# Performance work log

Measured on AMD Instinct MI355X. Metric: run time of the kernel, lower is better.

Reference implementation:

```python
import jax, jax.numpy as jnp
import numpy as np

EPS = 1e-5

def _ln(x, g, b):
    m = jnp.mean(x, -1, keepdims=True)
    v = jnp.mean((x - m) ** 2, -1, keepdims=True)
    return (x - m) * jax.lax.rsqrt(v + EPS) * g + b

def _lstm(x, Wih, Whh, bih, bhh):
    # x: [B, T, D]; torch gate order i, f, g, o; h0 = c0 = 0
    B = x.shape[0]
    H = Whh.shape[1]
    h0 = jnp.zeros((B, H), x.dtype)
    c0 = jnp.zeros((B, H), x.dtype)
    bias = bih + bhh
    def step(carry, xt):
        h, c = carry
        gates = xt @ Wih.T + h @ Whh.T + bias  # [B, 4H]
        i, f, g, o = jnp.split(gates, 4, axis=-1)
        c = jax.nn.sigmoid(f) * c + jax.nn.sigmoid(i) * jnp.tanh(g)
        h = jax.nn.sigmoid(o) * jnp.tanh(c)
        return (h, c), h
    _, hs = jax.lax.scan(step, (h0, c0), jnp.swapaxes(x, 0, 1))
    return jnp.swapaxes(hs, 0, 1)  # [B, T, H]

def setup_inputs() -> dict:
    key = jax.random.key(0)
    ks = jax.random.split(key, 20)
    N, C, F, T = 4, 64, 256, 256
    D, H = 128, 32  # LSTM in/out
    s = 0.05
    inp = {
        "inputs": jax.random.normal(ks[0], (N, C, F, T, 2), jnp.float32),
        "ln1_g": jnp.ones((D,), jnp.float32), "ln1_b": jnp.zeros((D,), jnp.float32),
        "Wih_q": s * jax.random.normal(ks[1], (4 * H, D), jnp.float32),
        "Whh_q": s * jax.random.normal(ks[2], (4 * H, H), jnp.float32),
        "bih_q": s * jax.random.normal(ks[3], (4 * H,), jnp.float32),
        "bhh_q": s * jax.random.normal(ks[4], (4 * H,), jnp.float32),
        "Wih_k": s * jax.random.normal(ks[5], (4 * H, D), jnp.float32),
        "Whh_k": s * jax.random.normal(ks[6], (4 * H, H), jnp.float32),
        "bih_k": s * jax.random.normal(ks[7], (4 * H,), jnp.float32),
        "bhh_k": s * jax.random.normal(ks[8], (4 * H,), jnp.float32),
        "Wih_v": s * jax.random.normal(ks[9], (4 * H, D), jnp.float32),
        "Whh_v": s * jax.random.normal(ks[10], (4 * H, H), jnp.float32),
        "bih_v": s * jax.random.normal(ks[11], (4 * H,), jnp.float32),
        "bhh_v": s * jax.random.normal(ks[12], (4 * H,), jnp.float32),
        "ln2_g": jnp.ones((H,), jnp.float32), "ln2_b": jnp.zeros((H,), jnp.float32),
        "Wr": s * jax.random.normal(ks[13], (C, H // 2), jnp.float32),
        "br": s * jax.random.normal(ks[14], (C,), jnp.float32),
        "Wi": s * jax.random.normal(ks[15], (C, H // 2), jnp.float32),
        "bi": s * jax.random.normal(ks[16], (C,), jnp.float32),
        "ln3_g": jnp.ones((C,), jnp.float32), "ln3_b": jnp.zeros((C,), jnp.float32),
        "prelu_a": jnp.full((1,), 0.25, jnp.float32),
    }
    return inp

def reference(inputs, ln1_g, ln1_b,
              Wih_q, Whh_q, bih_q, bhh_q,
              Wih_k, Whh_k, bih_k, bhh_k,
              Wih_v, Whh_v, bih_v, bhh_v,
              ln2_g, ln2_b, Wr, br, Wi, bi,
              ln3_g, ln3_b, prelu_a):
    N, C, F, T, ri = inputs.shape
    # [N,C,F,T,2] -> [N*F, T, C, 2] -> concat real/imag -> [N*F, T, 2C]
    x4 = jnp.transpose(inputs, (0, 2, 3, 1, 4)).reshape(N * F, T, C, ri)
    x = jnp.concatenate([x4[..., 0], x4[..., 1]], axis=-1)  # [B, T, 128]
    # Self_Attention_T_RICAT (single head)
    xn = _ln(x, ln1_g, ln1_b)
    q = _lstm(xn, Wih_q, Whh_q, bih_q, bhh_q)  # [B, T, 32]
    k = _lstm(xn, Wih_k, Whh_k, bih_k, bhh_k)
    v = _lstm(xn, Wih_v, Whh_v, bih_v, bhh_v)
    energy = jnp.einsum('btf,bsf->bts', q, k) / 4.0  # / 16**0.5
    mask = jnp.tril(jnp.ones((T, T), x.dtype))
    attn = jax.nn.softmax(energy * mask, axis=-1)  # multiplicative mask, as in source
    wv = jnp.einsum('bts,bsf->btf', attn, v)  # [B, T, 32]
    out = _ln(wv, ln2_g, ln2_b)
    # complex-valued linear fusion
    xr, xi = jnp.split(out, 2, axis=-1)  # [B, T, 16] each
    lr_r = xr @ Wr.T + br
    li_i = xi @ Wi.T + bi
    lr_i = xi @ Wr.T + br
    li_r = xr @ Wi.T + bi
    out_real = (lr_r - li_i).reshape(N, F, T, C).transpose(0, 3, 1, 2)  # [N,C,F,T]
    out_imag = (lr_i + li_r).reshape(N, F, T, C).transpose(0, 3, 1, 2)
    outs = jnp.stack([out_real, out_imag], axis=-1)  # [N,C,F,T,2]
    outs_t = jnp.swapaxes(outs, 1, 4)  # [N,2,F,T,C]
    outs = jnp.swapaxes(_ln(outs_t, ln3_g, ln3_b), 1, 4)
    outs = jnp.where(outs >= 0, outs, prelu_a[0] * outs)  # PReLU (eval mode, dropout=identity)
    return outs + inputs
```

## Files before the change

### kernel.cpp

```cpp
#include <hip/hip_runtime.h>
#include <hip/hip_bf16.h>
#include <stddef.h>


typedef __bf16 bf16x8 __attribute__((ext_vector_type(8)));
typedef float f32x4 __attribute__((ext_vector_type(4)));

__device__ __forceinline__ ushort f2bf(float x) {
    uint u = __builtin_bit_cast(uint, x);
    uint r = (u + 0x7fffu + ((u >> 16) & 1u)) >> 16;
    return (ushort)r;
}

__device__ __forceinline__ float fsig(float x) {
    return __builtin_amdgcn_rcpf(1.f + __expf(-x));
}
__device__ __forceinline__ float ftanh(float x) {
    return 1.f - 2.f * __builtin_amdgcn_rcpf(__expf(2.f * x) + 1.f);
}
__device__ __forceinline__ float wredsum(float v) {
#pragma unroll
    for (int off = 32; off; off >>= 1) v += __shfl_xor(v, off);
    return v;
}
__device__ __forceinline__ float hredsum(float v) {
#pragma unroll
    for (int off = 16; off; off >>= 1) v += __shfl_xor(v, off);
    return v;
}

__global__ __launch_bounds__(256) void k_prep(const float* __restrict__ in,
                                              const float* __restrict__ g1,
                                              const float* __restrict__ b1,
                                              ushort* __restrict__ xn) {
    __shared__ float xl[32][129];
    const int n = blockIdx.z, f = blockIdx.y, t0 = blockIdx.x * 32;
    const int tid = threadIdx.x;
    const int c = tid >> 2, q = tid & 3;
    const float* src = in + ((size_t)(n * 64 + c) * 256 + f) * 512 + t0 * 2 + q * 16;
#pragma unroll
    for (int e = 0; e < 4; ++e) {
        float4 v4 = *(const float4*)(src + e * 4);
        int dt = q * 8 + e * 2;
        xl[dt][c]          = v4.x;
        xl[dt][c + 64]     = v4.y;
        xl[dt + 1][c]      = v4.z;
        xl[dt + 1][c + 64] = v4.w;
    }
    __syncthreads();
    const int lane = tid & 63, w = tid >> 6;
    const int b = n * 256 + f;
#pragma unroll 1
    for (int r = 0; r < 8; ++r) {
        int dt = w * 8 + r;
        float a = xl[dt][lane], bb = xl[dt][lane + 64];
        float s = wredsum(a + bb);
        float mean = s * 0.0078125f;
        float da = a - mean, db = bb - mean;
        float var = wredsum(da * da + db * db) * 0.0078125f;
        float inv = __builtin_amdgcn_rsqf(var + 1e-5f);
        size_t base = ((size_t)b * 256 + (t0 + dt)) * 128;
        xn[base + lane]      = f2bf(da * inv * g1[lane] + b1[lane]);
        xn[base + lane + 64] = f2bf(db * inv * g1[lane + 64] + b1[lane + 64]);
    }
}

__global__ __launch_bounds__(256) void k_gemm(const ushort* __restrict__ xn,
                                              const float* __restrict__ Wq,
                                              const float* __restrict__ Wk,
                                              const float* __restrict__ Wv,
                                              const float* __restrict__ bihq, const float* __restrict__ bhhq,
                                              const float* __restrict__ bihk, const float* __restrict__ bhhk,
                                              const float* __restrict__ bihv, const float* __restrict__ bhhv,
                                              ushort* __restrict__ gx) {
    __shared__ ushort a_lds[128 * 136];
    __shared__ ushort w_lds[128 * 136];
    const int tid = threadIdx.x;
    const int m0 = blockIdx.x * 128;

#pragma unroll
    for (int p = 0; p < 8; ++p) {
        int idx = p * 256 + tid;
        int r = idx >> 4, c = idx & 15;
        *(uint4*)&a_lds[r * 136 + c * 8] =
            *(const uint4*)(xn + (size_t)(m0 + r) * 128 + c * 8);
    }

    const int w = tid >> 6, lane = tid & 63;
    const int wr = w >> 1, wc = w & 1;
    const int row16 = lane & 15, koct = lane >> 4;

#pragma unroll 1
    for (int l = 0; l < 3; ++l) {
        const float* W   = (l == 0) ? Wq   : (l == 1) ? Wk   : Wv;
        const float* bih = (l == 0) ? bihq : (l == 1) ? bihk : bihv;
        const float* bhh = (l == 0) ? bhhq : (l == 1) ? bhhk : bhhv;
        __syncthreads();
#pragma unroll
        for (int p = 0; p < 8; ++p) {
            int idx = p * 256 + tid;
            int r = idx >> 4, c = idx & 15;
            const float* wp = W + (size_t)r * 128 + c * 8;
            float4 wa = *(const float4*)wp;
            float4 wb = *(const float4*)(wp + 4);
            union { ushort u[8]; uint4 v; } pk;
            pk.u[0] = f2bf(wa.x); pk.u[1] = f2bf(wa.y); pk.u[2] = f2bf(wa.z); pk.u[3] = f2bf(wa.w);
            pk.u[4] = f2bf(wb.x); pk.u[5] = f2bf(wb.y); pk.u[6] = f2bf(wb.z); pk.u[7] = f2bf(wb.w);
            *(uint4*)&w_lds[r * 136 + c * 8] = pk.v;
        }
        __syncthreads();

        f32x4 acc[4][4];
#pragma unroll
        for (int mi = 0; mi < 4; ++mi)
#pragma unroll
            for (int ni = 0; ni < 4; ++ni) acc[mi][ni] = (f32x4){0.f, 0.f, 0.f, 0.f};

#pragma unroll
        for (int ki = 0; ki < 4; ++ki) {
            bf16x8 af[4], bfr[4];
#pragma unroll
            for (int mi = 0; mi < 4; ++mi)
                af[mi] = *(const bf16x8*)&a_lds[(wr * 64 + mi * 16 + row16) * 136 + ki * 32 + koct * 8];
#pragma unroll
            for (int ni = 0; ni < 4; ++ni)
                bfr[ni] = *(const bf16x8*)&w_lds[(wc * 64 + ni * 16 + row16) * 136 + ki * 32 + koct * 8];
#pragma unroll
            for (int mi = 0; mi < 4; ++mi)
#pragma unroll
                for (int ni = 0; ni < 4; ++ni)
                    acc[mi][ni] = __builtin_amdgcn_mfma_f32_16x16x32_bf16(af[mi], bfr[ni], acc[mi][ni], 0, 0, 0);
        }

#pragma unroll
        for (int ni = 0; ni < 4; ++ni) {
            int g = wc * 64 + ni * 16 + row16;
            float bsv = bih[g] + bhh[g];
            int j = g & 31, gi = g >> 5;
            int s = j * 4 + gi;
#pragma unroll
            for (int mi = 0; mi < 4; ++mi)
#pragma unroll
                for (int q = 0; q < 4; ++q) {
                    size_t m = (size_t)m0 + wr * 64 + mi * 16 + koct * 4 + q;
                    gx[m * 384 + l * 128 + s] = f2bf(acc[mi][ni][q] + bsv);
                }
        }
    }
}

__global__ __launch_bounds__(128, 1) void k_lstm(const ushort* __restrict__ gx,
                                                 const float* __restrict__ Whq,
                                                 const float* __restrict__ Whk,
                                                 const float* __restrict__ Whv,
                                                 ushort* __restrict__ qkv) {
    __shared__ ushort H[2][16][40];
    const int tid = threadIdx.x;
    const int w = tid >> 6, lane = tid & 63;
    const int r16 = lane & 15, koct = lane >> 4;
    const int l = blockIdx.x >> 6, bgrp = blockIdx.x & 63;
    const int b = bgrp * 16 + r16;
    const float* Wh = (l == 0) ? Whq : (l == 1) ? Whk : Whv;

    bf16x8 wf[4];
#pragma unroll
    for (int gg = 0; gg < 4; ++gg) {
        int g = 4 * w + gg;
        int jA = 8 * (r16 >> 2) + g;
        int giA = r16 & 3;
        const float* wp = Wh + (size_t)(giA * 32 + jA) * 32 + koct * 8;
        float4 wa = *(const float4*)wp;
        float4 wb = *(const float4*)(wp + 4);
        union { ushort u[8]; bf16x8 v; } pk;
        pk.u[0] = f2bf(wa.x); pk.u[1] = f2bf(wa.y); pk.u[2] = f2bf(wa.z); pk.u[3] = f2bf(wa.w);
        pk.u[4] = f2bf(wb.x); pk.u[5] = f2bf(wb.y); pk.u[6] = f2bf(wb.z); pk.u[7] = f2bf(wb.w);
        wf[gg] = pk.v;
    }

    const ushort* gp = gx + (size_t)b * 98304 + l * 128 + koct * 32 + w * 16;
    uint4 pf[4][2];
#pragma unroll
    for (int tt = 0; tt < 4; ++tt) {
        pf[tt][0] = *(const uint4*)(gp + (size_t)tt * 384);
        pf[tt][1] = *(const uint4*)(gp + (size_t)tt * 384 + 8);
    }

    for (int i = tid; i < 320; i += 128) ((uint*)&H[0][0][0])[i] = 0;
    __syncthreads();

    float cst[4] = {0.f, 0.f, 0.f, 0.f};
    ushort* outp = qkv + ((size_t)(l * 1024 + b)) * 8192 + koct * 8 + w * 4;

#pragma unroll 4
    for (int t = 0; t < 256; ++t) {
        const int sl = t & 3;
        const int p = t & 1;
        bf16x8 hf = *(const bf16x8*)&H[p][r16][koct * 8];

        uint u[8];
        u[0] = pf[sl][0].x; u[1] = pf[sl][0].y; u[2] = pf[sl][0].z; u[3] = pf[sl][0].w;
        u[4] = pf[sl][1].x; u[5] = pf[sl][1].y; u[6] = pf[sl][1].z; u[7] = pf[sl][1].w;
        pf[sl][0] = *(const uint4*)(gp + (size_t)(t + 4) * 384);
        pf[sl][1] = *(const uint4*)(gp + (size_t)(t + 4) * 384 + 8);

        f32x4 acc[4];
#pragma unroll
        for (int gg = 0; gg < 4; ++gg)
#pragma unroll
            for (int q = 0; q < 4; ++q) {
                int v = gg * 4 + q;
                uint w32 = u[v >> 1];
                acc[gg][q] = __builtin_bit_cast(float, (v & 1) ? (w32 & 0xffff0000u) : (w32 << 16));
            }
#pragma unroll
        for (int gg = 0; gg < 4; ++gg)
            acc[gg] = __builtin_amdgcn_mfma_f32_16x16x32_bf16(wf[gg], hf, acc[gg], 0, 0, 0);

        float hv[4];
#pragma unroll
        for (int gg = 0; gg < 4; ++gg) {
            float gi = acc[gg][0], gf = acc[gg][1], gg2 = acc[gg][2], go = acc[gg][3];
            float cN = fsig(gf) * cst[gg] + fsig(gi) * ftanh(gg2);
            cst[gg] = cN;
            hv[gg] = fsig(go) * ftanh(cN);
        }
        uint2 hp;
        __asm__ volatile("v_cvt_pk_bf16_f32 %0, %1, %2" : "=v"(hp.x) : "v"(hv[0]), "v"(hv[1]));
        __asm__ volatile("v_cvt_pk_bf16_f32 %0, %1, %2" : "=v"(hp.y) : "v"(hv[2]), "v"(hv[3]));
        *(uint2*)&H[p ^ 1][r16][koct * 8 + w * 4] = hp;
        *(uint2*)(outp + (size_t)t * 32) = hp;
        __syncthreads();
    }
}

__global__ __launch_bounds__(256) void k_attn(const ushort* __restrict__ qkvb,
                                              float* __restrict__ wvout) {
    __shared__ ushort k_sw[256 * 32];
    __shared__ ushort vt_sw[32 * 256];
    __shared__ ushort p_sw[4][16 * 256];
    const int tid = threadIdx.x, w = tid >> 6, lane = tid & 63;
    const int b = blockIdx.x;
    const ushort* qb = qkvb + (size_t)b * 8192;
    const ushort* kb = qkvb + 8388608 + (size_t)b * 8192;
    const ushort* vb = qkvb + 16777216 + (size_t)b * 8192;
#pragma unroll
    for (int p = 0; p < 4; ++p) {
        int idx = p * 256 + tid;
        int s = idx >> 2, cc = idx & 3;
        uint4 kv = *(const uint4*)(kb + s * 32 + cc * 8);
        int cK = cc ^ ((s >> 1) & 3);
        *(uint4*)&k_sw[s * 32 + cK * 8] = kv;
        uint4 vv = *(const uint4*)(vb + s * 32 + cc * 8);
        union { uint4 v; ushort u[8]; } un; un.v = vv;
#pragma unroll
        for (int e = 0; e < 8; ++e) {
            int row = cc * 8 + e;
            vt_sw[row * 256 + (((s >> 3) ^ (row & 7)) << 3) + (s & 7)] = un.u[e];
        }
    }
    __syncthreads();
    const int r16 = lane & 15, koct = lane >> 4;
    ushort* pw = p_sw[w];
    bf16x8 qf[4];
#pragma unroll
    for (int i = 0; i < 4; ++i) {
        int t = (w * 4 + i) * 16 + r16;
        qf[i] = *(const bf16x8*)(qb + t * 32 + koct * 8);
    }
#pragma unroll 1
    for (int i = 0; i < 4; ++i) {
        const int tb = (w * 4 + i) * 16;
        f32x4 acc[16];
#pragma unroll
        for (int st = 0; st < 16; ++st) acc[st] = (f32x4){0.f, 0.f, 0.f, 0.f};
#pragma unroll
        for (int st = 0; st < 16; ++st) {
            int s = st * 16 + r16;
            int cK = koct ^ ((s >> 1) & 3);
            bf16x8 kf = *(const bf16x8*)&k_sw[s * 32 + cK * 8];
            acc[st] = __builtin_amdgcn_mfma_f32_16x16x32_bf16(qf[i], kf, acc[st], 0, 0, 0);
        }
        float mx[4] = {-1e30f, -1e30f, -1e30f, -1e30f};
#pragma unroll
        for (int st = 0; st < 16; ++st) {
            int s = st * 16 + r16;
#pragma unroll
            for (int q = 0; q < 4; ++q) {
                int t = tb + koct * 4 + q;
                float v = (s <= t) ? acc[st][q] * 0.25f : 0.f;
                acc[st][q] = v;
                mx[q] = fmaxf(mx[q], v);
            }
        }
#pragma unroll
        for (int off = 1; off < 16; off <<= 1)
#pragma unroll
            for (int q = 0; q < 4; ++q) mx[q] = fmaxf(mx[q], __shfl_xor(mx[q], off));
        float sm[4] = {0.f, 0.f, 0.f, 0.f};
#pragma unroll
        for (int st = 0; st < 16; ++st)
#pragma unroll
            for (int q = 0; q < 4; ++q) {
                float p = __expf(acc[st][q] - mx[q]);
                acc[st][q] = p; sm[q] += p;
            }
#pragma unroll
        for (int off = 1; off < 16; off <<= 1)
#pragma unroll
            for (int q = 0; q < 4; ++q) sm[q] += __shfl_xor(sm[q], off);
        float rs[4];
#pragma unroll
        for (int q = 0; q < 4; ++q) rs[q] = __builtin_amdgcn_rcpf(sm[q]);
#pragma unroll
        for (int st = 0; st < 16; ++st) {
            int schunk = st * 2 + (r16 >> 3), sl = r16 & 7;
#pragma unroll
            for (int q = 0; q < 4; ++q) {
                int tl = koct * 4 + q;
                pw[tl * 256 + ((schunk ^ (tl & 7)) << 3) + sl] = f2bf(acc[st][q] * rs[q]);
            }
        }
        __asm__ volatile("s_waitcnt lgkmcnt(0)" ::: "memory");
        f32x4 oa[2];
        oa[0] = (f32x4){0.f, 0.f, 0.f, 0.f};
        oa[1] = (f32x4){0.f, 0.f, 0.f, 0.f};
#pragma unroll
        for (int ks = 0; ks < 8; ++ks) {
            int kc = ks * 4 + koct;
            bf16x8 pa = *(const bf16x8*)&pw[r16 * 256 + ((kc ^ (r16 & 7)) << 3)];
#pragma unroll
            for (int n = 0; n < 2; ++n) {
                int row = n * 16 + r16;
                bf16x8 vf = *(const bf16x8*)&vt_sw[row * 256 + ((kc ^ (row & 7)) << 3)];
                oa[n] = __builtin_amdgcn_mfma_f32_16x16x32_bf16(pa, vf, oa[n], 0, 0, 0);
            }
        }
#pragma unroll
        for (int n = 0; n < 2; ++n)
#pragma unroll
            for (int q = 0; q < 4; ++q)
                wvout[((size_t)b * 256 + tb + koct * 4 + q) * 32 + n * 16 + r16] = oa[n][q];
    }
}

__global__ __launch_bounds__(256) void k_post(const float* __restrict__ wv,
                                              const float* __restrict__ in,
                                              const float* __restrict__ g2,
                                              const float* __restrict__ b2,
                                              const float* __restrict__ Wr,
                                              const float* __restrict__ br,
                                              const float* __restrict__ Wi,
                                              const float* __restrict__ bi,
                                              const float* __restrict__ g3,
                                              const float* __restrict__ b3,
                                              const float* __restrict__ pa,
                                              float* __restrict__ outp) {
    __shared__ float xv[32][36];
    __shared__ float out_s[64][65];
    const int tid = threadIdx.x;
    const int n = blockIdx.z, f = blockIdx.y, t0 = blockIdx.x * 32;
    const int b = n * 256 + f;
    const int lane = tid & 63, w = tid >> 6;
    const int r16 = lane & 15, koct = lane >> 4;
    const int tt = w & 1, ri = w >> 1;

    for (int idx = tid; idx < 1024; idx += 256) {
        int dt = idx >> 5, j = idx & 31;
        xv[dt][j] = wv[((size_t)b * 256 + t0 + dt) * 32 + j];
    }

    bf16x8 bfr[4];
    float bias_v[4], g3v[4], b3v[4];
    const int kofs = (koct < 2) ? koct * 8 : (koct - 2) * 8;
#pragma unroll
    for (int ct = 0; ct < 4; ++ct) {
        int c = ct * 16 + r16;
        const float* srcW = (ri == 0) ? ((koct < 2) ? Wr : Wi)
                                      : ((koct < 2) ? Wi : Wr);
        float sgn = (ri == 0 && koct >= 2) ? -1.f : 1.f;
        float4 wa = *(const float4*)(srcW + c * 16 + kofs);
        float4 wb = *(const float4*)(srcW + c * 16 + kofs + 4);
        union { ushort u[8]; bf16x8 v; } pk;
        pk.u[0] = f2bf(sgn * wa.x); pk.u[1] = f2bf(sgn * wa.y);
        pk.u[2] = f2bf(sgn * wa.z); pk.u[3] = f2bf(sgn * wa.w);
        pk.u[4] = f2bf(sgn * wb.x); pk.u[5] = f2bf(sgn * wb.y);
        pk.u[6] = f2bf(sgn * wb.z); pk.u[7] = f2bf(sgn * wb.w);
        bfr[ct] = pk.v;
        bias_v[ct] = (ri == 0) ? (br[c] - bi[c]) : (br[c] + bi[c]);
        g3v[ct] = g3[c];
        b3v[ct] = b3[c];
    }
    const float alpha = pa[0];
    __syncthreads();

#pragma unroll 1
    for (int r = 0; r < 4; ++r) {
        int dt = w * 8 + r * 2 + (lane >> 5);
        int j = lane & 31;
        float v = xv[dt][j];
        float mean = hredsum(v) * 0.03125f;
        float d = v - mean;
        float var = hredsum(d * d) * 0.03125f;
        float inv = __builtin_amdgcn_rsqf(var + 1e-5f);
        xv[dt][j] = d * inv * g2[j] + b2[j];
    }
    __syncthreads();

    const float* xrow = &xv[tt * 16 + r16][koct * 8];
    float4 a0 = *(const float4*)xrow;
    float4 a1 = *(const float4*)(xrow + 4);
    uint4 ap;
    __asm__ volatile("v_cvt_pk_bf16_f32 %0, %1, %2" : "=v"(ap.x) : "v"(a0.x), "v"(a0.y));
    __asm__ volatile("v_cvt_pk_bf16_f32 %0, %1, %2" : "=v"(ap.y) : "v"(a0.z), "v"(a0.w));
    __asm__ volatile("v_cvt_pk_bf16_f32 %0, %1, %2" : "=v"(ap.z) : "v"(a1.x), "v"(a1.y));
    __asm__ volatile("v_cvt_pk_bf16_f32 %0, %1, %2" : "=v"(ap.w) : "v"(a1.z), "v"(a1.w));
    bf16x8 af = __builtin_bit_cast(bf16x8, ap);

    f32x4 acc[4];
#pragma unroll
    for (int ct = 0; ct < 4; ++ct) {
        acc[ct] = (f32x4){0.f, 0.f, 0.f, 0.f};
        acc[ct] = __builtin_amdgcn_mfma_f32_16x16x32_bf16(af, bfr[ct], acc[ct], 0, 0, 0);
    }

    float val[4][4];
    float s[4] = {0.f, 0.f, 0.f, 0.f}, sq[4] = {0.f, 0.f, 0.f, 0.f};
#pragma unroll
    for (int ct = 0; ct < 4; ++ct)
#pragma unroll
        for (int q = 0; q < 4; ++q) {
            float v = acc[ct][q] + bias_v[ct];
            val[ct][q] = v;
            s[q] += v;
            sq[q] += v * v;
        }
#pragma unroll
    for (int off = 1; off < 16; off <<= 1)
#pragma unroll
        for (int q = 0; q < 4; ++q) {
            s[q]  += __shfl_xor(s[q], off);
            sq[q] += __shfl_xor(sq[q], off);
        }
#pragma unroll
    for (int q = 0; q < 4; ++q) {
        float m = s[q] * 0.015625f;
        float var = fmaxf(sq[q] * 0.015625f - m * m, 0.f);
        float inv = __builtin_amdgcn_rsqf(var + 1e-5f);
        int t2 = (tt * 16 + koct * 4 + q) * 2 + ri;
#pragma unroll
        for (int ct = 0; ct < 4; ++ct) {
            float nv = (val[ct][q] - m) * inv * g3v[ct] + b3v[ct];
            nv = (nv >= 0.f) ? nv : alpha * nv;
            out_s[ct * 16 + r16][t2] = nv;
        }
    }
    __syncthreads();

    const int cc = tid >> 2, q = tid & 3;
    size_t base = ((size_t)(n * 64 + cc) * 256 + f) * 512 + t0 * 2 + q * 16;
#pragma unroll
    for (int e = 0; e < 4; ++e) {
        float4 iv = *(const float4*)(in + base + e * 4);
        int k0 = q * 16 + e * 4;
        float4 ov;
        ov.x = out_s[cc][k0]     + iv.x;
        ov.y = out_s[cc][k0 + 1] + iv.y;
        ov.z = out_s[cc][k0 + 2] + iv.z;
        ov.w = out_s[cc][k0 + 3] + iv.w;
        *(float4*)(outp + base + e * 4) = ov;
    }
}

extern "C" void kernel_launch(void* const* d_in, const int* in_sizes, int n_in,
                              void* d_out, int out_size, void* d_ws, size_t ws_size,
                              hipStream_t stream) {
    const float* in   = (const float*)d_in[0];
    const float* g1   = (const float*)d_in[1];
    const float* b1   = (const float*)d_in[2];
    const float* Wq   = (const float*)d_in[3];
    const float* Whq  = (const float*)d_in[4];
    const float* bihq = (const float*)d_in[5];
    const float* bhhq = (const float*)d_in[6];
    const float* Wk   = (const float*)d_in[7];
    const float* Whk  = (const float*)d_in[8];
    const float* bihk = (const float*)d_in[9];
    const float* bhhk = (const float*)d_in[10];
    const float* Wv   = (const float*)d_in[11];
    const float* Whv  = (const float*)d_in[12];
    const float* bihv = (const float*)d_in[13];
    const float* bhhv = (const float*)d_in[14];
    const float* g2   = (const float*)d_in[15];
    const float* b2   = (const float*)d_in[16];
    const float* Wr   = (const float*)d_in[17];
    const float* br   = (const float*)d_in[18];
    const float* Wi   = (const float*)d_in[19];
    const float* bi   = (const float*)d_in[20];
    const float* g3   = (const float*)d_in[21];
    const float* b3   = (const float*)d_in[22];
    const float* pa   = (const float*)d_in[23];
    float* outp = (float*)d_out;

    ushort* gxb  = (ushort*)d_ws;
    ushort* xnb  = (ushort*)((char*)d_ws + 201326592);
    ushort* qkvb = (ushort*)((char*)d_ws + 268435456);
    float*  wvb  = (float*)((char*)d_ws + 318767104);

    k_prep<<<dim3(8, 256, 4), dim3(256), 0, stream>>>(in, g1, b1, xnb);
    k_gemm<<<dim3(2048), dim3(256), 0, stream>>>(xnb, Wq, Wk, Wv,
                                                 bihq, bhhq, bihk, bhhk, bihv, bhhv, gxb);
    k_lstm<<<dim3(192), dim3(128), 0, stream>>>(gxb, Whq, Whk, Whv, qkvb);
    k_attn<<<dim3(1024), dim3(256), 0, stream>>>(qkvb, wvb);
    k_post<<<dim3(8, 256, 4), dim3(256), 0, stream>>>(wvb, in, g2, b2,
                                                      Wr, br, Wi, bi, g3, b3, pa, outp);
}
```

Measured before the change: 474.6 us.

## Run each LSTM block as a single wave, keeping hidden state in registers

The recurrent LSTM kernel drops from two waves per block to one. Each lane now handles eight gate groups instead of four, and the gate permutation in the input-projection GEMM is reordered so that a lane's MFMA output lines up directly with the B-operand layout for the next step. This lets the hidden state stay in registers and removes the per-timestep LDS write, LDS read and __syncthreads from the serial loop. In exchange each wave does twice the MFMA and transcendental work per step, with more registers and fewer waves in flight.

```diff
diff --git a/kernel.cpp b/kernel.cpp
--- a/kernel.cpp
+++ b/kernel.cpp
@@ -137,7 +137,7 @@
             int g = wc * 64 + ni * 16 + row16;
             float bsv = bih[g] + bhh[g];
             int j = g & 31, gi = g >> 5;
-            int s = j * 4 + gi;
+            int s = (j >> 3) * 32 + (j & 7) * 4 + gi;
 #pragma unroll
             for (int mi = 0; mi < 4; ++mi)
 #pragma unroll
@@ -149,87 +149,89 @@
     }
 }
 
-__global__ __launch_bounds__(128, 1) void k_lstm(const ushort* __restrict__ gx,
-                                                 const float* __restrict__ Whq,
-                                                 const float* __restrict__ Whk,
-                                                 const float* __restrict__ Whv,
-                                                 ushort* __restrict__ qkv) {
-    __shared__ ushort H[2][16][40];
-    const int tid = threadIdx.x;
-    const int w = tid >> 6, lane = tid & 63;
+__global__ __launch_bounds__(64, 1) void k_lstm(const ushort* __restrict__ gx,
+                                                const float* __restrict__ Whq,
+                                                const float* __restrict__ Whk,
+                                                const float* __restrict__ Whv,
+                                                ushort* __restrict__ qkv) {
+    const int lane = threadIdx.x & 63;
     const int r16 = lane & 15, koct = lane >> 4;
     const int l = blockIdx.x >> 6, bgrp = blockIdx.x & 63;
     const int b = bgrp * 16 + r16;
     const float* Wh = (l == 0) ? Whq : (l == 1) ? Whk : Whv;
 
-    bf16x8 wf[4];
-#pragma unroll
-    for (int gg = 0; gg < 4; ++gg) {
-        int g = 4 * w + gg;
-        int jA = 8 * (r16 >> 2) + g;
-        int giA = r16 & 3;
+    bf16x8 wf[8];
+#pragma unroll
+    for (int g = 0; g < 8; ++g) {
+        int P = g * 16 + r16;
+        int jA = 8 * ((P >> 2) & 3) + (P >> 4);
+        int giA = P & 3;
         const float* wp = Wh + (size_t)(giA * 32 + jA) * 32 + koct * 8;
         float4 wa = *(const float4*)wp;
         float4 wb = *(const float4*)(wp + 4);
         union { ushort u[8]; bf16x8 v; } pk;
         pk.u[0] = f2bf(wa.x); pk.u[1] = f2bf(wa.y); pk.u[2] = f2bf(wa.z); pk.u[3] = f2bf(wa.w);
         pk.u[4] = f2bf(wb.x); pk.u[5] = f2bf(wb.y); pk.u[6] = f2bf(wb.z); pk.u[7] = f2bf(wb.w);
-        wf[gg] = pk.v;
-    }
-
-    const ushort* gp = gx + (size_t)b * 98304 + l * 128 + koct * 32 + w * 16;
-    uint4 pf[4][2];
-#pragma unroll
-    for (int tt = 0; tt < 4; ++tt) {
-        pf[tt][0] = *(const uint4*)(gp + (size_t)tt * 384);
-        pf[tt][1] = *(const uint4*)(gp + (size_t)tt * 384 + 8);
-    }
-
-    for (int i = tid; i < 320; i += 128) ((uint*)&H[0][0][0])[i] = 0;
-    __syncthreads();
-
-    float cst[4] = {0.f, 0.f, 0.f, 0.f};
-    ushort* outp = qkv + ((size_t)(l * 1024 + b)) * 8192 + koct * 8 + w * 4;
+        wf[g] = pk.v;
+    }
+
+    const ushort* gp = gx + (size_t)b * 98304 + l * 128 + koct * 32;
+    uint4 pf[4][4];
+#pragma unroll
+    for (int tt = 0; tt < 4; ++tt)
+#pragma unroll
+        for (int i = 0; i < 4; ++i)
+            pf[tt][i] = *(const uint4*)(gp + (size_t)tt * 384 + i * 8);
+
+    float cst[8] = {0.f, 0.f, 0.f, 0.f, 0.f, 0.f, 0.f, 0.f};
+    uint4 z4 = make_uint4(0, 0, 0, 0);
+    bf16x8 hf = __builtin_bit_cast(bf16x8, z4);
+    ushort* outp = qkv + ((size_t)(l * 1024 + b)) * 8192 + koct * 8;
 
 #pragma unroll 4
     for (int t = 0; t < 256; ++t) {
         const int sl = t & 3;
-        const int p = t & 1;
-        bf16x8 hf = *(const bf16x8*)&H[p][r16][koct * 8];
-
-        uint u[8];
-        u[0] = pf[sl][0].x; u[1] = pf[sl][0].y; u[2] = pf[sl][0].z; u[3] = pf[sl][0].w;
-        u[4] = pf[sl][1].x; u[5] = pf[sl][1].y; u[6] = pf[sl][1].z; u[7] = pf[sl][1].w;
-        pf[sl][0] = *(const uint4*)(gp + (size_t)(t + 4) * 384);
-        pf[sl][1] = *(const uint4*)(gp + (size_t)(t + 4) * 384 + 8);
-
-        f32x4 acc[4];
-#pragma unroll
-        for (int gg = 0; gg < 4; ++gg)
+        uint u[16];
+#pragma unroll
+        for (int i = 0; i < 4; ++i) {
+            u[4 * i]     = pf[sl][i].x;
+            u[4 * i + 1] = pf[sl][i].y;
+            u[4 * i + 2] = pf[sl][i].z;
+            u[4 * i + 3] = pf[sl][i].w;
+        }
+        int tn = (t + 4 < 256) ? t + 4 : 255;
+#pragma unroll
+        for (int i = 0; i < 4; ++i)
+            pf[sl][i] = *(const uint4*)(gp + (size_t)tn * 384 + i * 8);
+
+        f32x4 acc[8];
+#pragma unroll
+        for (int g = 0; g < 8; ++g)
 #pragma unroll
             for (int q = 0; q < 4; ++q) {
-                int v = gg * 4 + q;
+                int v = g * 4 + q;
                 uint w32 = u[v >> 1];
-                acc[gg][q] = __builtin_bit_cast(float, (v & 1) ? (w32 & 0xffff0000u) : (w32 << 16));
+                acc[g][q] = __builtin_bit_cast(float, (v & 1) ? (w32 & 0xffff0000u) : (w32 << 16));
             }
 #pragma unroll
-        for (int gg = 0; gg < 4; ++gg)
-            acc[gg] = __builtin_amdgcn_mfma_f32_16x16x32_bf16(wf[gg], hf, acc[gg], 0, 0, 0);
-
-        float hv[4];
-#pragma unroll
-        for (int gg = 0; gg < 4; ++gg) {
-            float gi = acc[gg][0], gf = acc[gg][1], gg2 = acc[gg][2], go = acc[gg][3];
-            float cN = fsig(gf) * cst[gg] + fsig(gi) * ftanh(gg2);
-            cst[gg] = cN;
-            hv[gg] = fsig(go) * ftanh(cN);
-        }
-        uint2 hp;
+        for (int g = 0; g < 8; ++g)
+            acc[g] = __builtin_amdgcn_mfma_f32_16x16x32_bf16(wf[g], hf, acc[g], 0, 0, 0);
+
+        float hv[8];
+#pragma unroll
+        for (int g = 0; g < 8; ++g) {
+            float gi = acc[g][0], gf = acc[g][1], gg = acc[g][2], go = acc[g][3];
+            float cN = fsig(gf) * cst[g] + fsig(gi) * ftanh(gg);
+            cst[g] = cN;
+            hv[g] = fsig(go) * ftanh(cN);
+        }
+        uint4 hp;
         __asm__ volatile("v_cvt_pk_bf16_f32 %0, %1, %2" : "=v"(hp.x) : "v"(hv[0]), "v"(hv[1]));
         __asm__ volatile("v_cvt_pk_bf16_f32 %0, %1, %2" : "=v"(hp.y) : "v"(hv[2]), "v"(hv[3]));
-        *(uint2*)&H[p ^ 1][r16][koct * 8 + w * 4] = hp;
-        *(uint2*)(outp + (size_t)t * 32) = hp;
-        __syncthreads();
+        __asm__ volatile("v_cvt_pk_bf16_f32 %0, %1, %2" : "=v"(hp.z) : "v"(hv[4]), "v"(hv[5]));
+        __asm__ volatile("v_cvt_pk_bf16_f32 %0, %1, %2" : "=v"(hp.w) : "v"(hv[6]), "v"(hv[7]));
+        hf = __builtin_bit_cast(bf16x8, hp);
+        *(uint4*)(outp + (size_t)t * 32) = hp;
     }
 }
 
@@ -508,7 +510,7 @@
     k_prep<<<dim3(8, 256, 4), dim3(256), 0, stream>>>(in, g1, b1, xnb);
     k_gemm<<<dim3(2048), dim3(256), 0, stream>>>(xnb, Wq, Wk, Wv,
                                                  bihq, bhhq, bihk, bhhk, bihv, bhhv, gxb);
-    k_lstm<<<dim3(192), dim3(128), 0, stream>>>(gxb, Whq, Whk, Whv, qkvb);
+    k_lstm<<<dim3(192), dim3(64), 0, stream>>>(gxb, Whq, Whk, Whv, qkvb);
     k_attn<<<dim3(1024), dim3(256), 0, stream>>>(qkvb, wvb);
     k_post<<<dim3(8, 256, 4), dim3(256), 0, stream>>>(wvb, in, g2, b2,
                                                       Wr, br, Wi, bi, g3, b3, pa, outp);
```

After: 558.0 us. +17.6%, slower.

## Stage LSTM gate inputs via async global-to-LDS loads, double-buffered per 4 steps

Applied to the files above, without the earlier changes.

The LSTM recurrence kernel stops prefetching precomputed gate inputs into registers with per-step global loads. It now issues global_load_lds copies for the next 4 timesteps into a double-buffered shared-memory stage, and each step reads its inputs from LDS. The output store of h is delayed by one step so the global write is off the critical path before the barrier. Shared memory use grows and correctness now depends on the per-step barrier also covering the async LDS fills, since no explicit vmcnt wait is issued.

```diff
diff --git a/kernel.cpp b/kernel.cpp
--- a/kernel.cpp
+++ b/kernel.cpp
@@ -155,6 +155,7 @@
                                                  const float* __restrict__ Whv,
                                                  ushort* __restrict__ qkv) {
     __shared__ ushort H[2][16][40];
+    __shared__ ushort gstage[2][2][4][2][512];
     const int tid = threadIdx.x;
     const int w = tid >> 6, lane = tid & 63;
     const int r16 = lane & 15, koct = lane >> 4;
@@ -177,60 +178,78 @@
         wf[gg] = pk.v;
     }
 
-    const ushort* gp = gx + (size_t)b * 98304 + l * 128 + koct * 32 + w * 16;
-    uint4 pf[4][2];
-#pragma unroll
-    for (int tt = 0; tt < 4; ++tt) {
-        pf[tt][0] = *(const uint4*)(gp + (size_t)tt * 384);
-        pf[tt][1] = *(const uint4*)(gp + (size_t)tt * 384 + 8);
-    }
+    const char* gsrc = (const char*)(gx + (size_t)b * 98304 + l * 128 + koct * 32 + w * 16);
+
+#pragma unroll
+    for (int t4 = 0; t4 < 4; ++t4)
+#pragma unroll
+        for (int i = 0; i < 2; ++i)
+            __builtin_amdgcn_global_load_lds(
+                (const __attribute__((address_space(1))) uint*)(gsrc + t4 * 768 + i * 16),
+                (__attribute__((address_space(3))) uint*)((char*)&gstage[0][w][t4][i][0]),
+                16, 0, 0);
 
     for (int i = tid; i < 320; i += 128) ((uint*)&H[0][0][0])[i] = 0;
     __syncthreads();
 
     float cst[4] = {0.f, 0.f, 0.f, 0.f};
     ushort* outp = qkv + ((size_t)(l * 1024 + b)) * 8192 + koct * 8 + w * 4;
-
-#pragma unroll 4
-    for (int t = 0; t < 256; ++t) {
-        const int sl = t & 3;
-        const int p = t & 1;
-        bf16x8 hf = *(const bf16x8*)&H[p][r16][koct * 8];
-
-        uint u[8];
-        u[0] = pf[sl][0].x; u[1] = pf[sl][0].y; u[2] = pf[sl][0].z; u[3] = pf[sl][0].w;
-        u[4] = pf[sl][1].x; u[5] = pf[sl][1].y; u[6] = pf[sl][1].z; u[7] = pf[sl][1].w;
-        pf[sl][0] = *(const uint4*)(gp + (size_t)(t + 4) * 384);
-        pf[sl][1] = *(const uint4*)(gp + (size_t)(t + 4) * 384 + 8);
-
-        f32x4 acc[4];
-#pragma unroll
-        for (int gg = 0; gg < 4; ++gg)
-#pragma unroll
-            for (int q = 0; q < 4; ++q) {
-                int v = gg * 4 + q;
-                uint w32 = u[v >> 1];
-                acc[gg][q] = __builtin_bit_cast(float, (v & 1) ? (w32 & 0xffff0000u) : (w32 << 16));
+    uint2 hprev = make_uint2(0, 0);
+
+#pragma unroll 1
+    for (int c = 0; c < 64; ++c) {
+        const int cur = c & 1;
+        if (c < 63) {
+            const char* gs = gsrc + (size_t)(c + 1) * 3072;
+#pragma unroll
+            for (int t4 = 0; t4 < 4; ++t4)
+#pragma unroll
+                for (int i = 0; i < 2; ++i)
+                    __builtin_amdgcn_global_load_lds(
+                        (const __attribute__((address_space(1))) uint*)(gs + t4 * 768 + i * 16),
+                        (__attribute__((address_space(3))) uint*)((char*)&gstage[cur ^ 1][w][t4][i][0]),
+                        16, 0, 0);
+        }
+#pragma unroll
+        for (int t4 = 0; t4 < 4; ++t4) {
+            const int t = c * 4 + t4;
+            const int p = t & 1;
+            if (t > 0) *(uint2*)(outp + (size_t)(t - 1) * 32) = hprev;
+            bf16x8 hf = *(const bf16x8*)&H[p][r16][koct * 8];
+            uint4 ga = *(const uint4*)&gstage[cur][w][t4][0][lane * 8];
+            uint4 gb = *(const uint4*)&gstage[cur][w][t4][1][lane * 8];
+            uint u[8] = {ga.x, ga.y, ga.z, ga.w, gb.x, gb.y, gb.z, gb.w};
+
+            f32x4 acc[4];
+#pragma unroll
+            for (int gg = 0; gg < 4; ++gg)
+#pragma unroll
+                for (int q = 0; q < 4; ++q) {
+                    int v = gg * 4 + q;
+                    uint w32 = u[v >> 1];
+                    acc[gg][q] = __builtin_bit_cast(float, (v & 1) ? (w32 & 0xffff0000u) : (w32 << 16));
+                }
+#pragma unroll
+            for (int gg = 0; gg < 4; ++gg)
+                acc[gg] = __builtin_amdgcn_mfma_f32_16x16x32_bf16(wf[gg], hf, acc[gg], 0, 0, 0);
+
+            float hv[4];
+#pragma unroll
+            for (int gg = 0; gg < 4; ++gg) {
+                float gi = acc[gg][0], gf = acc[gg][1], gg2 = acc[gg][2], go = acc[gg][3];
+                float cN = fsig(gf) * cst[gg] + fsig(gi) * ftanh(gg2);
+                cst[gg] = cN;
+                hv[gg] = fsig(go) * ftanh(cN);
             }
-#pragma unroll
-        for (int gg = 0; gg < 4; ++gg)
-            acc[gg] = __builtin_amdgcn_mfma_f32_16x16x32_bf16(wf[gg], hf, acc[gg], 0, 0, 0);
-
-        float hv[4];
-#pragma unroll
-        for (int gg = 0; gg < 4; ++gg) {
-            float gi = acc[gg][0], gf = acc[gg][1], gg2 = acc[gg][2], go = acc[gg][3];
-            float cN = fsig(gf) * cst[gg] + fsig(gi) * ftanh(gg2);
-            cst[gg] = cN;
-            hv[gg] = fsig(go) * ftanh(cN);
-        }
-        uint2 hp;
-        __asm__ volatile("v_cvt_pk_bf16_f32 %0, %1, %2" : "=v"(hp.x) : "v"(hv[0]), "v"(hv[1]));
-        __asm__ volatile("v_cvt_pk_bf16_f32 %0, %1, %2" : "=v"(hp.y) : "v"(hv[2]), "v"(hv[3]));
-        *(uint2*)&H[p ^ 1][r16][koct * 8 + w * 4] = hp;
-        *(uint2*)(outp + (size_t)t * 32) = hp;
-        __syncthreads();
-    }
+            uint2 hp;
+            __asm__ volatile("v_cvt_pk_bf16_f32 %0, %1, %2" : "=v"(hp.x) : "v"(hv[0]), "v"(hv[1]));
+            __asm__ volatile("v_cvt_pk_bf16_f32 %0, %1, %2" : "=v"(hp.y) : "v"(hv[2]), "v"(hv[3]));
+            *(uint2*)&H[p ^ 1][r16][koct * 8 + w * 4] = hp;
+            hprev = hp;
+            __syncthreads();
+        }
+    }
+    *(uint2*)(outp + (size_t)255 * 32) = hprev;
 }
 
 __global__ __launch_bounds__(256) void k_attn(const ushort* __restrict__ qkvb,
```

New measurement: 519.5 us. 1.09x slower.
